# Performance work log

Hardware: AMD Instinct MI355X
Metric: run time of the kernel (lower is better)

Reference implementation:

```python
import jax, jax.numpy as jnp
import numpy as np

N, M, C = 32768, 8192, 128
K = 3            # number of interpolation neighbors (PointNet++/RepSurf FP)
EPS_BN = 1e-5    # torch BatchNorm1d default eps
EPS_D = 1e-8     # RepSurf dist_recip eps


def setup_inputs() -> dict:
    key = jax.random.key(0)
    ks = jax.random.split(key, 16)
    s = 0.05
    inp = {
        "pos1": jax.random.normal(ks[0], (N, 3), jnp.float32),
        "pos2": jax.random.normal(ks[1], (M, 3), jnp.float32),
        "feat2": jax.random.normal(ks[2], (M, C), jnp.float32),
    }
    # MLP stack [128,128,128]: Linear + BatchNorm1d (gamma/beta) per layer
    for i in range(3):
        inp[f"W{i}"] = jax.random.normal(ks[3 + i], (C, C), jnp.float32) * s
        inp[f"b{i}"] = jnp.zeros((C,), jnp.float32)
        inp[f"g{i}"] = jnp.ones((C,), jnp.float32)
        inp[f"be{i}"] = jnp.zeros((C,), jnp.float32)
    return inp


def _lin_bn_relu(x, W, b, g, be):
    # Linear -> BatchNorm1d (training-mode batch stats, biased var) -> ReLU
    y = x @ W.T + b
    m = y.mean(axis=0)
    v = y.var(axis=0)
    return jax.nn.relu((y - m) * jax.lax.rsqrt(v + EPS_BN) * g + be)


def reference(pos1, pos2, feat2, W0, b0, g0, be0, W1, b1, g1, be1, W2, b2, g2, be2):
    # squared pairwise distances [N, M] (memory-bound: 1 GB fp32)
    d = ((pos1 ** 2).sum(-1, keepdims=True)
         + (pos2 ** 2).sum(-1)[None, :]
         - 2.0 * (pos1 @ pos2.T))
    neg_d, idx = jax.lax.top_k(-d, K)          # 3 nearest neighbors
    dk = jnp.maximum(-neg_d, 0.0)              # [N, K] squared dists
    w = 1.0 / (dk + EPS_D)
    w = w / w.sum(-1, keepdims=True)           # inverse-distance weights
    # gather neighbor features and interpolate: [N, K, C] -> [N, C]
    interp = jnp.einsum('nkc,nk->nc', feat2[idx], w)
    x = _lin_bn_relu(interp, W0, b0, g0, be0)
    x = _lin_bn_relu(x, W1, b1, g1, be1)
    x = _lin_bn_relu(x, W2, b2, g2, be2)
    return x
```

## Files before the change

### kernel.cpp

```cpp
#include <hip/hip_runtime.h>
#include <math.h>

#define NQ 32768
#define MC 8192
#define CC 128
#define EPS_BN 1e-5f
#define EPS_D  1e-8

#define DBL_BIG 1e300
#define IDX_BIG 0x7fffffff

#define QB  64
#define TB  512
#define NW  8
#define HM  (MC / 2)
#define SLCW (HM / NW)
#define KMASK 0xFFFFE000u
#define IMASK 0x1FFFu
#define NSURV 64
#define KNN_B ((NQ / QB) * 2)
#define GEMM_B (NQ / 64)
#define NGRP 8

typedef __attribute__((ext_vector_type(8))) short bf16x8;
typedef __attribute__((ext_vector_type(4))) float floatx4;
typedef unsigned short ushort_t;

__device__ __forceinline__ unsigned bf16pair(float a, float b) {
    unsigned ua = __float_as_uint(a); ua = (ua + 0x7FFFu + ((ua >> 16) & 1u)) >> 16;
    unsigned ub = __float_as_uint(b); ub = (ub + 0x7FFFu + ((ub >> 16) & 1u)) >> 16;
    return ua | (ub << 16);
}
__device__ __forceinline__ ushort_t bf16one(float a) {
    unsigned ua = __float_as_uint(a);
    return (ushort_t)((ua + 0x7FFFu + ((ua >> 16) & 1u)) >> 16);
}
__device__ __forceinline__ float bflo(unsigned u) { return __uint_as_float(u << 16); }
__device__ __forceinline__ float bfhi(unsigned u) { return __uint_as_float(u & 0xFFFF0000u); }

__device__ __forceinline__ void ins4(float& k0, float& k1, float& k2, float& k3, float x) {
    const float n0 = fminf(k0, x);
    const float n1 = __builtin_amdgcn_fmed3f(k0, k1, x);
    const float n2 = __builtin_amdgcn_fmed3f(k1, k2, x);
    const float n3 = __builtin_amdgcn_fmed3f(k2, k3, x);
    k0 = n0; k1 = n1; k2 = n2; k3 = n3;
}

__device__ __forceinline__ float mkk(float nx, float ny, float nz, float hp,
                                     float4 c, unsigned j) {
    float t = c.w + hp;
    t = fmaf(nz, c.z, t);
    t = fmaf(ny, c.y, t);
    t = fmaf(nx, c.x, t);
    return __uint_as_float((__float_as_uint(t) & KMASK) | j);
}

__global__ __launch_bounds__(TB) void pack_kernel(const float* __restrict__ pos2,
                                                  float4* __restrict__ pos2pk) {
    const int c0 = blockIdx.x * (MC / 8);
#pragma unroll
    for (int c = c0 + threadIdx.x; c < c0 + MC / 8; c += TB) {
        const float x = pos2[c * 3 + 0];
        const float y = pos2[c * 3 + 1];
        const float z = pos2[c * 3 + 2];
        float4 v;
        v.x = x; v.y = y; v.z = z;
        v.w = 0.5f * fmaf(x, x, fmaf(y, y, z * z));
        pos2pk[c] = v;
    }
}

__global__ __launch_bounds__(TB) void knn_kernel(const float* __restrict__ pos1,
                                                 const float4* __restrict__ pos2pk,
                                                 unsigned* __restrict__ skeys,
                                                 const float* __restrict__ W0,
                                                 const float* __restrict__ W1,
                                                 const float* __restrict__ W2,
                                                 ushort_t* __restrict__ Wbf,
                                                 float* __restrict__ stats) {
    __shared__ unsigned skl[QB][33];

    if (blockIdx.x >= KNN_B) {
        const int pb = blockIdx.x - KNN_B;
        const int f = pb * TB + threadIdx.x;
        const float* Ws[3] = {W0, W1, W2};
#pragma unroll
        for (int l = 0; l < 3; ++l) {
            const float4 v = ((const float4*)Ws[l])[f];
            unsigned* dst = (unsigned*)(Wbf + (size_t)l * CC * CC);
            dst[f * 2 + 0] = bf16pair(v.x, v.y);
            dst[f * 2 + 1] = bf16pair(v.z, v.w);
        }
        if (pb == 0)
            for (int i = threadIdx.x; i < 3 * NGRP * 256; i += TB) stats[i] = 0.f;
        return;
    }

    const int half = blockIdx.x & 1;
    const int bq   = blockIdx.x >> 1;
    const int ln = threadIdx.x & 63;
    const int wvu = __builtin_amdgcn_readfirstlane((int)(threadIdx.x >> 6));
    const int q  = bq * QB + ln;

    const float px = pos1[q * 3 + 0];
    const float py = pos1[q * 3 + 1];
    const float pz = pos1[q * 3 + 2];
    const float nx = -px, ny = -py, nz = -pz;
    const float hp = 0.5f * fmaf(px, px, fmaf(py, py, pz * pz));

    const int jb = half * HM + wvu * SLCW;
    const float4* cp = pos2pk + jb;

    const float KINIT = __uint_as_float(0x7F000000u);
    float k0 = KINIT, k1 = KINIT, k2 = KINIT, k3 = KINIT;

#pragma unroll 4
    for (int gi = 0; gi < SLCW / 4; ++gi) {
        const float4 c0 = cp[gi * 4 + 0];
        const float4 c1 = cp[gi * 4 + 1];
        const float4 c2 = cp[gi * 4 + 2];
        const float4 c3 = cp[gi * 4 + 3];
        const unsigned j0 = (unsigned)(jb + gi * 4);
        ins4(k0, k1, k2, k3, mkk(nx, ny, nz, hp, c0, j0 + 0));
        ins4(k0, k1, k2, k3, mkk(nx, ny, nz, hp, c1, j0 + 1));
        ins4(k0, k1, k2, k3, mkk(nx, ny, nz, hp, c2, j0 + 2));
        ins4(k0, k1, k2, k3, mkk(nx, ny, nz, hp, c3, j0 + 3));
    }

    skl[ln][wvu * 4 + 0] = __float_as_uint(k0);
    skl[ln][wvu * 4 + 1] = __float_as_uint(k1);
    skl[ln][wvu * 4 + 2] = __float_as_uint(k2);
    skl[ln][wvu * 4 + 3] = __float_as_uint(k3);
    __syncthreads();

#pragma unroll
    for (int t = threadIdx.x * 4; t < threadIdx.x * 4 + 4; ++t) {
        const int ql = t >> 5, slot = t & 31;
        skeys[(size_t)(bq * QB + ql) * NSURV + half * 32 + slot] = skl[ql][slot];
    }
}

template <int MODE>
__global__ __launch_bounds__(256) void gemm_mfma(const void* __restrict__ Xsrc_,
                                                 const unsigned* __restrict__ skeys,
                                                 const float* __restrict__ pos1,
                                                 const float* __restrict__ pos2,
                                                 const float* __restrict__ statsIn,
                                                 const float* __restrict__ gIn,
                                                 const float* __restrict__ beIn,
                                                 const ushort_t* __restrict__ Wb,
                                                 const float* __restrict__ bias,
                                                 ushort_t* __restrict__ Y,
                                                 float* __restrict__ statsOut) {
    __shared__ __align__(16) short xa[64][136];
    __shared__ __align__(16) short wb[128][136];
    __shared__ float blk_s[CC], blk_q[CC];
    __shared__ float sc_l[CC], sh_l[CC];

    const int row0 = blockIdx.x * 64;

    if constexpr (MODE == 0) {
        const float* feat2 = (const float*)Xsrc_;
        __shared__ int   lidx[QB][3];
        __shared__ float lw[QB][3];
        {
            double* rrd = (double*)&xa[0][0];
            int*    rri = (int*)&wb[0][0];
            const int ql = threadIdx.x >> 2;
            const int pp = threadIdx.x & 3;
            const int qg = row0 + ql;
            const double qx = (double)pos1[qg * 3 + 0];
            const double qy = (double)pos1[qg * 3 + 1];
            const double qz = (double)pos1[qg * 3 + 2];
            double b0 = DBL_BIG, b1 = DBL_BIG, b2 = DBL_BIG;
            int    j0 = IDX_BIG, j1 = IDX_BIG, j2 = IDX_BIG;
            const uint4* kp = (const uint4*)(skeys + (size_t)qg * NSURV + pp * 16);
#pragma unroll
            for (int gi = 0; gi < 4; ++gi) {
                const uint4 kk = kp[gi];
                const unsigned ks[4] = {kk.x, kk.y, kk.z, kk.w};
#pragma unroll
                for (int u = 0; u < 4; ++u) {
                    const int id = (int)(ks[u] & IMASK);
                    const double x = (double)pos2[id * 3 + 0];
                    const double y = (double)pos2[id * 3 + 1];
                    const double z = (double)pos2[id * 3 + 2];
                    const double ax = qx - x, ay = qy - y, az = qz - z;
                    const double d = ax * ax + ay * ay + az * az;
                    const bool l2 = (d < b2) || (d == b2 && id < j2);
                    if (l2) {
                        const bool l1 = (d < b1) || (d == b1 && id < j1);
                        const bool l0 = (d < b0) || (d == b0 && id < j0);
                        b2 = l1 ? b1 : d;              j2 = l1 ? j1 : id;
                        b1 = l1 ? (l0 ? b0 : d) : b1;  j1 = l1 ? (l0 ? j0 : id) : j1;
                        b0 = l0 ? d : b0;              j0 = l0 ? id : j0;
                    }
                }
            }
            const int base = (ql * 4 + pp) * 3;
            rrd[base + 0] = b0; rri[base + 0] = j0;
            rrd[base + 1] = b1; rri[base + 1] = j1;
            rrd[base + 2] = b2; rri[base + 2] = j2;
            __syncthreads();
            if (threadIdx.x < QB) {
                const int qq = threadIdx.x;
                double c0 = DBL_BIG, c1 = DBL_BIG, c2 = DBL_BIG;
                int    i0 = IDX_BIG, i1 = IDX_BIG, i2 = IDX_BIG;
#pragma unroll
                for (int s = 0; s < 12; ++s) {
                    const double d = rrd[qq * 12 + s];
                    const int   id = rri[qq * 12 + s];
                    const bool l2 = (d < c2) || (d == c2 && id < i2);
                    if (l2) {
                        const bool l1 = (d < c1) || (d == c1 && id < i1);
                        const bool l0 = (d < c0) || (d == c0 && id < i0);
                        c2 = l1 ? c1 : d;              i2 = l1 ? i1 : id;
                        c1 = l1 ? (l0 ? c0 : d) : c1;  i1 = l1 ? (l0 ? i0 : id) : i1;
                        c0 = l0 ? d : c0;              i0 = l0 ? id : i0;
                    }
                }
                const double r0 = 1.0 / (c0 + EPS_D);
                const double r1 = 1.0 / (c1 + EPS_D);
                const double r2 = 1.0 / (c2 + EPS_D);
                const double inv = 1.0 / (r0 + r1 + r2);
                lidx[qq][0] = i0; lidx[qq][1] = i1; lidx[qq][2] = i2;
                lw[qq][0] = (float)(r0 * inv);
                lw[qq][1] = (float)(r1 * inv);
                lw[qq][2] = (float)(r2 * inv);
            }
            __syncthreads();
        }
        if (threadIdx.x < CC) { blk_s[threadIdx.x] = 0.f; blk_q[threadIdx.x] = 0.f; }
#pragma unroll
        for (int e = threadIdx.x; e < 64 * 32; e += 256) {
            const int r = e >> 5, c4 = e & 31;
            const int i0 = lidx[r][0], i1 = lidx[r][1], i2 = lidx[r][2];
            const float w0 = lw[r][0], w1 = lw[r][1], w2 = lw[r][2];
            const float4 f0 = *(const float4*)&feat2[(size_t)i0 * CC + c4 * 4];
            const float4 f1 = *(const float4*)&feat2[(size_t)i1 * CC + c4 * 4];
            const float4 f2 = *(const float4*)&feat2[(size_t)i2 * CC + c4 * 4];
            float4 v;
            v.x = w0 * f0.x + w1 * f1.x + w2 * f2.x;
            v.y = w0 * f0.y + w1 * f1.y + w2 * f2.y;
            v.z = w0 * f0.z + w1 * f1.z + w2 * f2.z;
            v.w = w0 * f0.w + w1 * f1.w + w2 * f2.w;
            unsigned* dst = (unsigned*)&xa[r][0];
            dst[c4 * 2 + 0] = bf16pair(v.x, v.y);
            dst[c4 * 2 + 1] = bf16pair(v.z, v.w);
        }
    } else {
        const ushort_t* Xbf = (const ushort_t*)Xsrc_;
        if (threadIdx.x < CC) {
            const int c = threadIdx.x;
            float s = 0.f, q = 0.f;
#pragma unroll
            for (int gr = 0; gr < NGRP; ++gr) {
                s += statsIn[gr * 256 + c];
                q += statsIn[gr * 256 + CC + c];
            }
            const float m = s * (1.f / (float)NQ);
            const float v = fmaf(-m, m, q * (1.f / (float)NQ));
            const float rstd = rsqrtf(v + EPS_BN);
            const float scl = gIn[c] * rstd;
            sc_l[c] = scl;
            sh_l[c] = fmaf(-m, scl, beIn[c]);
            blk_s[c] = 0.f; blk_q[c] = 0.f;
        }
        __syncthreads();
#pragma unroll
        for (int e = threadIdx.x; e < 64 * 16; e += 256) {
            const int r = e >> 4, c8 = e & 15;
            const uint4 u = *(const uint4*)&Xbf[(size_t)(row0 + r) * CC + c8 * 8];
            const float4 s0 = *(const float4*)&sc_l[c8 * 8];
            const float4 s1 = *(const float4*)&sc_l[c8 * 8 + 4];
            const float4 h0 = *(const float4*)&sh_l[c8 * 8];
            const float4 h1 = *(const float4*)&sh_l[c8 * 8 + 4];
            const float v0 = fmaxf(fmaf(bflo(u.x), s0.x, h0.x), 0.f);
            const float v1 = fmaxf(fmaf(bfhi(u.x), s0.y, h0.y), 0.f);
            const float v2 = fmaxf(fmaf(bflo(u.y), s0.z, h0.z), 0.f);
            const float v3 = fmaxf(fmaf(bfhi(u.y), s0.w, h0.w), 0.f);
            const float v4 = fmaxf(fmaf(bflo(u.z), s1.x, h1.x), 0.f);
            const float v5 = fmaxf(fmaf(bfhi(u.z), s1.y, h1.y), 0.f);
            const float v6 = fmaxf(fmaf(bflo(u.w), s1.z, h1.z), 0.f);
            const float v7 = fmaxf(fmaf(bfhi(u.w), s1.w, h1.w), 0.f);
            uint4 o;
            o.x = bf16pair(v0, v1); o.y = bf16pair(v2, v3);
            o.z = bf16pair(v4, v5); o.w = bf16pair(v6, v7);
            *(uint4*)&xa[r][c8 * 8] = o;
        }
    }
#pragma unroll
    for (int e = threadIdx.x; e < 128 * 16; e += 256) {
        const int co = e >> 4, seg = e & 15;
        *(float4*)&wb[co][seg * 8] = *(const float4*)&Wb[(size_t)co * CC + seg * 8];
    }
    __syncthreads();

    const int lane = threadIdx.x & 63;
    const int wv = threadIdx.x >> 6;
    const int nn = lane & 15;
    const int quad = lane >> 4;

    floatx4 acc[8] = {};

    const short* arow = &xa[wv * 16 + nn][0];
#pragma unroll
    for (int ks = 0; ks < 4; ++ks) {
        const bf16x8 a = *(const bf16x8*)(arow + ks * 32 + quad * 8);
#pragma unroll
        for (int ct = 0; ct < 8; ++ct) {
            const bf16x8 b = *(const bf16x8*)(&wb[ct * 16 + nn][0] + ks * 32 + quad * 8);
            acc[ct] = __builtin_amdgcn_mfma_f32_16x16x32_bf16(a, b, acc[ct], 0, 0, 0);
        }
    }

#pragma unroll
    for (int ct = 0; ct < 8; ++ct) {
        const float bv = bias[ct * 16 + nn];
        float s = 0.f, qv = 0.f;
#pragma unroll
        for (int r = 0; r < 4; ++r) {
            acc[ct][r] += bv;
            s += acc[ct][r];
            qv = fmaf(acc[ct][r], acc[ct][r], qv);
        }
#pragma unroll
        for (int r = 0; r < 4; ++r)
            Y[(size_t)(row0 + wv * 16 + quad * 4 + r) * CC + ct * 16 + nn] = bf16one(acc[ct][r]);
        s += __shfl_xor(s, 16, 64); s += __shfl_xor(s, 32, 64);
        qv += __shfl_xor(qv, 16, 64); qv += __shfl_xor(qv, 32, 64);
        if (quad == 0) {
            atomicAdd(&blk_s[ct * 16 + nn], s);
            atomicAdd(&blk_q[ct * 16 + nn], qv);
        }
    }
    __syncthreads();
    {
        const int ch = threadIdx.x;
        const float v = (ch < CC) ? blk_s[ch] : blk_q[ch - CC];
        atomicAdd(&statsOut[(blockIdx.x & (NGRP - 1)) * 256 + ch], v);
    }
}

__global__ __launch_bounds__(256) void bn_final(const ushort_t* __restrict__ Y,
                                                const float* __restrict__ statsIn,
                                                const float* __restrict__ g,
                                                const float* __restrict__ be,
                                                float* __restrict__ out) {
    __shared__ float sc_l[CC], sh_l[CC];
    if (threadIdx.x < CC) {
        const int c = threadIdx.x;
        float s = 0.f, q = 0.f;
#pragma unroll
        for (int gr = 0; gr < NGRP; ++gr) {
            s += statsIn[gr * 256 + c];
            q += statsIn[gr * 256 + CC + c];
        }
        const float m = s * (1.f / (float)NQ);
        const float v = fmaf(-m, m, q * (1.f / (float)NQ));
        const float rstd = rsqrtf(v + EPS_BN);
        const float scl = g[c] * rstd;
        sc_l[c] = scl;
        sh_l[c] = fmaf(-m, scl, be[c]);
    }
    __syncthreads();
    const int base = blockIdx.x * 1024 + threadIdx.x;
#pragma unroll
    for (int it = 0; it < 4; ++it) {
        const int i8 = base + it * 256;
        const int c8 = (i8 & 15) * 8;
        const uint4 u = *(const uint4*)&Y[(size_t)i8 * 8];
        const float4 s0 = *(const float4*)&sc_l[c8];
        const float4 s1 = *(const float4*)&sc_l[c8 + 4];
        const float4 h0 = *(const float4*)&sh_l[c8];
        const float4 h1 = *(const float4*)&sh_l[c8 + 4];
        float4 o0, o1;
        o0.x = fmaxf(fmaf(bflo(u.x), s0.x, h0.x), 0.f);
        o0.y = fmaxf(fmaf(bfhi(u.x), s0.y, h0.y), 0.f);
        o0.z = fmaxf(fmaf(bflo(u.y), s0.z, h0.z), 0.f);
        o0.w = fmaxf(fmaf(bfhi(u.y), s0.w, h0.w), 0.f);
        o1.x = fmaxf(fmaf(bflo(u.z), s1.x, h1.x), 0.f);
        o1.y = fmaxf(fmaf(bfhi(u.z), s1.y, h1.y), 0.f);
        o1.z = fmaxf(fmaf(bflo(u.w), s1.z, h1.z), 0.f);
        o1.w = fmaxf(fmaf(bfhi(u.w), s1.w, h1.w), 0.f);
        ((float4*)out)[i8 * 2 + 0] = o0;
        ((float4*)out)[i8 * 2 + 1] = o1;
    }
}

extern "C" void kernel_launch(void* const* d_in, const int* in_sizes, int n_in,
                              void* d_out, int out_size, void* d_ws, size_t ws_size,
                              hipStream_t stream) {
    (void)in_sizes; (void)n_in; (void)out_size; (void)ws_size;

    const float* pos1  = (const float*)d_in[0];
    const float* pos2  = (const float*)d_in[1];
    const float* feat2 = (const float*)d_in[2];
    const float* Wl[3]  = {(const float*)d_in[3], (const float*)d_in[7],  (const float*)d_in[11]};
    const float* bl[3]  = {(const float*)d_in[4], (const float*)d_in[8],  (const float*)d_in[12]};
    const float* gl[3]  = {(const float*)d_in[5], (const float*)d_in[9],  (const float*)d_in[13]};
    const float* bel[3] = {(const float*)d_in[6], (const float*)d_in[10], (const float*)d_in[14]};

    float* ws = (float*)d_ws;
    ushort_t* B0 = (ushort_t*)ws;
    ushort_t* B1 = B0 + (size_t)NQ * CC;
    unsigned* skeys = (unsigned*)(B1 + (size_t)NQ * CC);
    float* stats = (float*)(skeys + (size_t)NQ * NSURV);
    ushort_t* Wbf = (ushort_t*)(stats + 3 * NGRP * 256);
    float4* pos2pk = (float4*)(Wbf + 3 * CC * CC);

    float* st0 = stats + 0 * NGRP * 256;
    float* st1 = stats + 1 * NGRP * 256;
    float* st2 = stats + 2 * NGRP * 256;

    pack_kernel<<<8, TB, 0, stream>>>(pos2, pos2pk);
    knn_kernel<<<KNN_B + 8, TB, 0, stream>>>(pos1, pos2pk, skeys,
                                             Wl[0], Wl[1], Wl[2], Wbf, stats);
    gemm_mfma<0><<<GEMM_B, 256, 0, stream>>>(feat2, skeys, pos1, pos2,
                                             nullptr, nullptr, nullptr,
                                             Wbf + 0 * CC * CC, bl[0], B0, st0);
    gemm_mfma<1><<<GEMM_B, 256, 0, stream>>>(B0, nullptr, nullptr, nullptr,
                                             st0, gl[0], bel[0],
                                             Wbf + 1 * CC * CC, bl[1], B1, st1);
    gemm_mfma<1><<<GEMM_B, 256, 0, stream>>>(B1, nullptr, nullptr, nullptr,
                                             st1, gl[1], bel[1],
                                             Wbf + 2 * CC * CC, bl[2], B0, st2);
    bn_final<<<GEMM_B, 256, 0, stream>>>(B0, st2, gl[2], bel[2], (float*)d_out);
}
```

Baseline: 211.7 us.

## Split KNN scan into four pieces with top-3 per wave and prefetching

The candidate scan is split across four blocks per query group with four waves each, and each wave keeps a top-3 list instead of top-4, so every key costs one fewer med3. The loop is restructured to double-buffer candidate loads in registers, and the survivor count drops from 64 to 48, which shrinks both the key writes and the fp64 refinement loop in the first GEMM. Cutting to three survivors per wave reduces the slack for errors from the truncated keys, so near-tied neighbours are more likely to be missed. The prefetch reads past the end of each slice, which is why four zero padding entries are added after pos2pk.

```diff
diff --git a/kernel.cpp b/kernel.cpp
--- a/kernel.cpp
+++ b/kernel.cpp
@@ -11,14 +11,15 @@
 #define IDX_BIG 0x7fffffff
 
 #define QB  64
-#define TB  512
-#define NW  8
-#define HM  (MC / 2)
-#define SLCW (HM / NW)
+#define TB  256
+#define NW  4
+#define PCE (MC / 4)
+#define SLCW (PCE / NW)
+#define NG  (SLCW / 4)
 #define KMASK 0xFFFFE000u
 #define IMASK 0x1FFFu
-#define NSURV 64
-#define KNN_B ((NQ / QB) * 2)
+#define NSURV 48
+#define KNN_B ((NQ / QB) * 4)
 #define GEMM_B (NQ / 64)
 #define NGRP 8
 
@@ -38,12 +39,11 @@
 __device__ __forceinline__ float bflo(unsigned u) { return __uint_as_float(u << 16); }
 __device__ __forceinline__ float bfhi(unsigned u) { return __uint_as_float(u & 0xFFFF0000u); }
 
-__device__ __forceinline__ void ins4(float& k0, float& k1, float& k2, float& k3, float x) {
+__device__ __forceinline__ void ins3(float& k0, float& k1, float& k2, float x) {
     const float n0 = fminf(k0, x);
     const float n1 = __builtin_amdgcn_fmed3f(k0, k1, x);
     const float n2 = __builtin_amdgcn_fmed3f(k1, k2, x);
-    const float n3 = __builtin_amdgcn_fmed3f(k2, k3, x);
-    k0 = n0; k1 = n1; k2 = n2; k3 = n3;
+    k0 = n0; k1 = n1; k2 = n2;
 }
 
 __device__ __forceinline__ float mkk(float nx, float ny, float nz, float hp,
@@ -52,7 +52,8 @@
     t = fmaf(nz, c.z, t);
     t = fmaf(ny, c.y, t);
     t = fmaf(nx, c.x, t);
-    return __uint_as_float((__float_as_uint(t) & KMASK) | j);
+    const unsigned u = (__float_as_uint(t) & KMASK) | (j & ~KMASK);
+    return __uint_as_float(u);
 }
 
 __global__ __launch_bounds__(TB) void pack_kernel(const float* __restrict__ pos2,
@@ -68,6 +69,10 @@
         v.w = 0.5f * fmaf(x, x, fmaf(y, y, z * z));
         pos2pk[c] = v;
     }
+    if (blockIdx.x == 0 && threadIdx.x < 4) {
+        float4 zf; zf.x = 0.f; zf.y = 0.f; zf.z = 0.f; zf.w = 0.f;
+        pos2pk[MC + threadIdx.x] = zf;
+    }
 }
 
 __global__ __launch_bounds__(TB) void knn_kernel(const float* __restrict__ pos1,
@@ -78,7 +83,7 @@
                                                  const float* __restrict__ W2,
                                                  ushort_t* __restrict__ Wbf,
                                                  float* __restrict__ stats) {
-    __shared__ unsigned skl[QB][33];
+    __shared__ unsigned skl[QB][13];
 
     if (blockIdx.x >= KNN_B) {
         const int pb = blockIdx.x - KNN_B;
@@ -96,8 +101,8 @@
         return;
     }
 
-    const int half = blockIdx.x & 1;
-    const int bq   = blockIdx.x >> 1;
+    const int piece = blockIdx.x & 3;
+    const int bq    = blockIdx.x >> 2;
     const int ln = threadIdx.x & 63;
     const int wvu = __builtin_amdgcn_readfirstlane((int)(threadIdx.x >> 6));
     const int q  = bq * QB + ln;
@@ -108,35 +113,43 @@
     const float nx = -px, ny = -py, nz = -pz;
     const float hp = 0.5f * fmaf(px, px, fmaf(py, py, pz * pz));
 
-    const int jb = half * HM + wvu * SLCW;
+    const int jb = piece * PCE + wvu * SLCW;
     const float4* cp = pos2pk + jb;
 
     const float KINIT = __uint_as_float(0x7F000000u);
-    float k0 = KINIT, k1 = KINIT, k2 = KINIT, k3 = KINIT;
-
-#pragma unroll 4
-    for (int gi = 0; gi < SLCW / 4; ++gi) {
-        const float4 c0 = cp[gi * 4 + 0];
-        const float4 c1 = cp[gi * 4 + 1];
-        const float4 c2 = cp[gi * 4 + 2];
-        const float4 c3 = cp[gi * 4 + 3];
-        const unsigned j0 = (unsigned)(jb + gi * 4);
-        ins4(k0, k1, k2, k3, mkk(nx, ny, nz, hp, c0, j0 + 0));
-        ins4(k0, k1, k2, k3, mkk(nx, ny, nz, hp, c1, j0 + 1));
-        ins4(k0, k1, k2, k3, mkk(nx, ny, nz, hp, c2, j0 + 2));
-        ins4(k0, k1, k2, k3, mkk(nx, ny, nz, hp, c3, j0 + 3));
-    }
-
-    skl[ln][wvu * 4 + 0] = __float_as_uint(k0);
-    skl[ln][wvu * 4 + 1] = __float_as_uint(k1);
-    skl[ln][wvu * 4 + 2] = __float_as_uint(k2);
-    skl[ln][wvu * 4 + 3] = __float_as_uint(k3);
+    float k0 = KINIT, k1 = KINIT, k2 = KINIT;
+
+#define LOADG(v0, v1, v2, v3, g) { v0 = cp[(g)*4+0]; v1 = cp[(g)*4+1]; \
+                                   v2 = cp[(g)*4+2]; v3 = cp[(g)*4+3]; }
+#define CONSG(v0, v1, v2, v3, g) { const unsigned j0 = (unsigned)(jb + (g)*4); \
+        ins3(k0, k1, k2, mkk(nx, ny, nz, hp, v0, j0 + 0)); \
+        ins3(k0, k1, k2, mkk(nx, ny, nz, hp, v1, j0 + 1)); \
+        ins3(k0, k1, k2, mkk(nx, ny, nz, hp, v2, j0 + 2)); \
+        ins3(k0, k1, k2, mkk(nx, ny, nz, hp, v3, j0 + 3)); }
+
+    float4 A0, A1, A2, A3, B0, B1, B2, B3;
+    LOADG(A0, A1, A2, A3, 0);
+    for (int g = 0; g < NG; g += 2) {
+        LOADG(B0, B1, B2, B3, g + 1);
+        CONSG(A0, A1, A2, A3, g);
+        LOADG(A0, A1, A2, A3, g + 2);
+        CONSG(B0, B1, B2, B3, g + 1);
+    }
+#undef LOADG
+#undef CONSG
+
+    skl[ln][wvu * 3 + 0] = __float_as_uint(k0);
+    skl[ln][wvu * 3 + 1] = __float_as_uint(k1);
+    skl[ln][wvu * 3 + 2] = __float_as_uint(k2);
     __syncthreads();
 
-#pragma unroll
-    for (int t = threadIdx.x * 4; t < threadIdx.x * 4 + 4; ++t) {
-        const int ql = t >> 5, slot = t & 31;
-        skeys[(size_t)(bq * QB + ql) * NSURV + half * 32 + slot] = skl[ql][slot];
+    {
+        const int ql = threadIdx.x >> 2;
+        const int sp = (threadIdx.x & 3) * 3;
+        unsigned* dst = &skeys[(size_t)(bq * QB + ql) * NSURV + piece * 12 + sp];
+        dst[0] = skl[ql][sp + 0];
+        dst[1] = skl[ql][sp + 1];
+        dst[2] = skl[ql][sp + 2];
     }
 }
 
@@ -174,9 +187,9 @@
             const double qz = (double)pos1[qg * 3 + 2];
             double b0 = DBL_BIG, b1 = DBL_BIG, b2 = DBL_BIG;
             int    j0 = IDX_BIG, j1 = IDX_BIG, j2 = IDX_BIG;
-            const uint4* kp = (const uint4*)(skeys + (size_t)qg * NSURV + pp * 16);
-#pragma unroll
-            for (int gi = 0; gi < 4; ++gi) {
+            const uint4* kp = (const uint4*)(skeys + (size_t)qg * NSURV + pp * 12);
+#pragma unroll
+            for (int gi = 0; gi < 3; ++gi) {
                 const uint4 kk = kp[gi];
                 const unsigned ks[4] = {kk.x, kk.y, kk.z, kk.w};
 #pragma unroll
@@ -414,8 +427,8 @@
     float* st2 = stats + 2 * NGRP * 256;
 
     pack_kernel<<<8, TB, 0, stream>>>(pos2, pos2pk);
-    knn_kernel<<<KNN_B + 8, TB, 0, stream>>>(pos1, pos2pk, skeys,
-                                             Wl[0], Wl[1], Wl[2], Wbf, stats);
+    knn_kernel<<<KNN_B + 16, TB, 0, stream>>>(pos1, pos2pk, skeys,
+                                              Wl[0], Wl[1], Wl[2], Wbf, stats);
     gemm_mfma<0><<<GEMM_B, 256, 0, stream>>>(feat2, skeys, pos1, pos2,
                                              nullptr, nullptr, nullptr,
                                              Wbf + 0 * CC * CC, bl[0], B0, st0);
```

After: 203.3 us. 1.04x faster.

## Compute KNN distance candidates with fp16 MFMA using hi/lo split coordinates

Applied to the files above, without the earlier changes.

Moves the brute-force distance computation in the KNN kernel from scalar FMA onto MFMA f16 16x16x32 instructions. Coordinates and half-norms are split into fp16 hi/lo parts so the dot-product expansion keeps near-fp32 accuracy. Each lane now keeps a top-3 instead of a top-4 survivor list, which cuts the surviving candidates per query from 64 to 24 and shrinks the double-precision refinement in the first GEMM stage. The risk is that the fp16 split loses enough precision that a true neighbor drops out of the survivors. The ptile fetch at t+2/t+3 on the last loop iteration also reads past the end of the half's tile range.

```diff
diff --git a/kernel.cpp b/kernel.cpp
--- a/kernel.cpp
+++ b/kernel.cpp
@@ -1,4 +1,5 @@
 #include <hip/hip_runtime.h>
+#include <hip/hip_fp16.h>
 #include <math.h>
 
 #define NQ 32768
@@ -11,18 +12,17 @@
 #define IDX_BIG 0x7fffffff
 
 #define QB  64
-#define TB  512
-#define NW  8
-#define HM  (MC / 2)
-#define SLCW (HM / NW)
+#define TB  256
+#define NTIL 256
 #define KMASK 0xFFFFE000u
 #define IMASK 0x1FFFu
-#define NSURV 64
+#define NSURV 24
 #define KNN_B ((NQ / QB) * 2)
 #define GEMM_B (NQ / 64)
 #define NGRP 8
 
 typedef __attribute__((ext_vector_type(8))) short bf16x8;
+typedef __attribute__((ext_vector_type(8))) _Float16 half8;
 typedef __attribute__((ext_vector_type(4))) float floatx4;
 typedef unsigned short ushort_t;
 
@@ -38,47 +38,51 @@
 __device__ __forceinline__ float bflo(unsigned u) { return __uint_as_float(u << 16); }
 __device__ __forceinline__ float bfhi(unsigned u) { return __uint_as_float(u & 0xFFFF0000u); }
 
-__device__ __forceinline__ void ins4(float& k0, float& k1, float& k2, float& k3, float x) {
+__device__ __forceinline__ void ins3(float& k0, float& k1, float& k2, float x) {
     const float n0 = fminf(k0, x);
     const float n1 = __builtin_amdgcn_fmed3f(k0, k1, x);
     const float n2 = __builtin_amdgcn_fmed3f(k1, k2, x);
-    const float n3 = __builtin_amdgcn_fmed3f(k2, k3, x);
-    k0 = n0; k1 = n1; k2 = n2; k3 = n3;
-}
-
-__device__ __forceinline__ float mkk(float nx, float ny, float nz, float hp,
-                                     float4 c, unsigned j) {
-    float t = c.w + hp;
-    t = fmaf(nz, c.z, t);
-    t = fmaf(ny, c.y, t);
-    t = fmaf(nx, c.x, t);
-    return __uint_as_float((__float_as_uint(t) & KMASK) | j);
-}
+    k0 = n0; k1 = n1; k2 = n2;
+}
+
+#define PK2(a, b) ((unsigned)__half_as_ushort(a) | ((unsigned)__half_as_ushort(b) << 16))
 
 __global__ __launch_bounds__(TB) void pack_kernel(const float* __restrict__ pos2,
-                                                  float4* __restrict__ pos2pk) {
-    const int c0 = blockIdx.x * (MC / 8);
-#pragma unroll
-    for (int c = c0 + threadIdx.x; c < c0 + MC / 8; c += TB) {
-        const float x = pos2[c * 3 + 0];
-        const float y = pos2[c * 3 + 1];
-        const float z = pos2[c * 3 + 2];
-        float4 v;
-        v.x = x; v.y = y; v.z = z;
-        v.w = 0.5f * fmaf(x, x, fmaf(y, y, z * z));
-        pos2pk[c] = v;
-    }
+                                                  uint4* __restrict__ ptile) {
+    const int c = blockIdx.x * TB + threadIdx.x;
+    const float x = pos2[c * 3 + 0];
+    const float y = pos2[c * 3 + 1];
+    const float z = pos2[c * 3 + 2];
+    const __half chx = __float2half(x); const float fchx = __half2float(chx);
+    const __half chy = __float2half(y); const float fchy = __half2float(chy);
+    const __half chz = __float2half(z); const float fchz = __half2float(chz);
+    const __half clx = __float2half(x - fchx);
+    const __half cly = __float2half(y - fchy);
+    const __half clz = __float2half(z - fchz);
+    const double X = (double)fchx + (double)__half2float(clx);
+    const double Y = (double)fchy + (double)__half2float(cly);
+    const double Z = (double)fchz + (double)__half2float(clz);
+    const double hc = 0.5 * (X * X + Y * Y + Z * Z);
+    const __half hchi = __float2half((float)hc);
+    const __half hclo = __float2half((float)(hc - (double)__half2float(hchi)));
+    const __half one = __float2half(1.0f);
+    uint4 a0, a1;
+    a0.x = PK2(chx, chy); a0.y = PK2(chz, clx); a0.z = PK2(cly, clz); a0.w = PK2(chx, chy);
+    a1.x = PK2(chz, clx); a1.y = PK2(cly, clz); a1.z = PK2(hchi, hclo); a1.w = PK2(one, one);
+    const int t = c >> 4, m = c & 15;
+    ptile[(size_t)t * 32 + m]      = a0;
+    ptile[(size_t)t * 32 + 16 + m] = a1;
 }
 
 __global__ __launch_bounds__(TB) void knn_kernel(const float* __restrict__ pos1,
-                                                 const float4* __restrict__ pos2pk,
+                                                 const uint4* __restrict__ ptile,
                                                  unsigned* __restrict__ skeys,
                                                  const float* __restrict__ W0,
                                                  const float* __restrict__ W1,
                                                  const float* __restrict__ W2,
                                                  ushort_t* __restrict__ Wbf,
                                                  float* __restrict__ stats) {
-    __shared__ unsigned skl[QB][33];
+    __shared__ __align__(16) ushort_t qext[QB][16];
 
     if (blockIdx.x >= KNN_B) {
         const int pb = blockIdx.x - KNN_B;
@@ -98,45 +102,89 @@
 
     const int half = blockIdx.x & 1;
     const int bq   = blockIdx.x >> 1;
-    const int ln = threadIdx.x & 63;
-    const int wvu = __builtin_amdgcn_readfirstlane((int)(threadIdx.x >> 6));
-    const int q  = bq * QB + ln;
-
-    const float px = pos1[q * 3 + 0];
-    const float py = pos1[q * 3 + 1];
-    const float pz = pos1[q * 3 + 2];
-    const float nx = -px, ny = -py, nz = -pz;
-    const float hp = 0.5f * fmaf(px, px, fmaf(py, py, pz * pz));
-
-    const int jb = half * HM + wvu * SLCW;
-    const float4* cp = pos2pk + jb;
+
+    if (threadIdx.x < QB) {
+        const int qq = bq * QB + threadIdx.x;
+        const float x = pos1[qq * 3 + 0];
+        const float y = pos1[qq * 3 + 1];
+        const float z = pos1[qq * 3 + 2];
+        const __half phx = __float2half(x); const float fphx = __half2float(phx);
+        const __half phy = __float2half(y); const float fphy = __half2float(phy);
+        const __half phz = __float2half(z); const float fphz = __half2float(phz);
+        const __half plx = __float2half(x - fphx);
+        const __half ply = __float2half(y - fphy);
+        const __half plz = __float2half(z - fphz);
+        const double X = (double)fphx + (double)__half2float(plx);
+        const double Y = (double)fphy + (double)__half2float(ply);
+        const double Z = (double)fphz + (double)__half2float(plz);
+        const double hp = 0.5 * (X * X + Y * Y + Z * Z);
+        const __half hphi = __float2half((float)hp);
+        const __half hplo = __float2half((float)(hp - (double)__half2float(hphi)));
+        const ushort_t SG = 0x8000u;
+        const ushort_t nx = (ushort_t)(__half_as_ushort(phx) ^ SG);
+        const ushort_t ny = (ushort_t)(__half_as_ushort(phy) ^ SG);
+        const ushort_t nz = (ushort_t)(__half_as_ushort(phz) ^ SG);
+        const ushort_t mx = (ushort_t)(__half_as_ushort(plx) ^ SG);
+        const ushort_t my = (ushort_t)(__half_as_ushort(ply) ^ SG);
+        const ushort_t mz = (ushort_t)(__half_as_ushort(plz) ^ SG);
+        const ushort_t on = __half_as_ushort(__float2half(1.0f));
+        ushort_t* e = &qext[threadIdx.x][0];
+        e[0] = nx; e[1] = ny; e[2] = nz; e[3] = nx; e[4]  = ny; e[5]  = nz;
+        e[6] = mx; e[7] = my; e[8] = mz; e[9] = mx; e[10] = my; e[11] = mz;
+        e[12] = on; e[13] = on;
+        e[14] = __half_as_ushort(hphi); e[15] = __half_as_ushort(hplo);
+    }
+    __syncthreads();
+
+    const int lane = threadIdx.x & 63;
+    const int wv   = threadIdx.x >> 6;
+    const int cc   = lane & 15;
+    const int g    = lane >> 4;
+
+    uint4 bqu = {0u, 0u, 0u, 0u};
+    if (g < 2) bqu = *(const uint4*)&qext[wv * 16 + cc][g * 8];
+    const half8 bqh = *(const half8*)&bqu;
+
+    const uint4* lp = ptile + (size_t)(half * NTIL) * 32 + ((g & 1) * 16 + cc);
+#define LD(t) lp[(size_t)(t) * 32]
 
     const float KINIT = __uint_as_float(0x7F000000u);
-    float k0 = KINIT, k1 = KINIT, k2 = KINIT, k3 = KINIT;
-
-#pragma unroll 4
-    for (int gi = 0; gi < SLCW / 4; ++gi) {
-        const float4 c0 = cp[gi * 4 + 0];
-        const float4 c1 = cp[gi * 4 + 1];
-        const float4 c2 = cp[gi * 4 + 2];
-        const float4 c3 = cp[gi * 4 + 3];
-        const unsigned j0 = (unsigned)(jb + gi * 4);
-        ins4(k0, k1, k2, k3, mkk(nx, ny, nz, hp, c0, j0 + 0));
-        ins4(k0, k1, k2, k3, mkk(nx, ny, nz, hp, c1, j0 + 1));
-        ins4(k0, k1, k2, k3, mkk(nx, ny, nz, hp, c2, j0 + 2));
-        ins4(k0, k1, k2, k3, mkk(nx, ny, nz, hp, c3, j0 + 3));
-    }
-
-    skl[ln][wvu * 4 + 0] = __float_as_uint(k0);
-    skl[ln][wvu * 4 + 1] = __float_as_uint(k1);
-    skl[ln][wvu * 4 + 2] = __float_as_uint(k2);
-    skl[ln][wvu * 4 + 3] = __float_as_uint(k3);
-    __syncthreads();
-
-#pragma unroll
-    for (int t = threadIdx.x * 4; t < threadIdx.x * 4 + 4; ++t) {
-        const int ql = t >> 5, slot = t & 31;
-        skeys[(size_t)(bq * QB + ql) * NSURV + half * 32 + slot] = skl[ql][slot];
+    float k0 = KINIT, k1 = KINIT, k2 = KINIT;
+    unsigned j0 = (unsigned)(half * 4096 + g * 4 + 0);
+    unsigned j1 = j0 + 1, j2 = j0 + 2, j3 = j0 + 3;
+    const floatx4 zc = {0.f, 0.f, 0.f, 0.f};
+
+#define KEYS(d) { \
+        unsigned u0 = (__float_as_uint(d[0]) & KMASK) | (j0 & ~KMASK); \
+        unsigned u1 = (__float_as_uint(d[1]) & KMASK) | (j1 & ~KMASK); \
+        unsigned u2 = (__float_as_uint(d[2]) & KMASK) | (j2 & ~KMASK); \
+        unsigned u3 = (__float_as_uint(d[3]) & KMASK) | (j3 & ~KMASK); \
+        ins3(k0, k1, k2, __uint_as_float(u0)); \
+        ins3(k0, k1, k2, __uint_as_float(u1)); \
+        ins3(k0, k1, k2, __uint_as_float(u2)); \
+        ins3(k0, k1, k2, __uint_as_float(u3)); \
+        j0 += 16; j1 += 16; j2 += 16; j3 += 16; }
+
+    uint4 afA = LD(0);
+    uint4 afB = LD(1);
+    for (int t = 0; t < NTIL; t += 2) {
+        const uint4 nA = LD(t + 2);
+        const floatx4 dA = __builtin_amdgcn_mfma_f32_16x16x32_f16(*(const half8*)&afA, bqh, zc, 0, 0, 0);
+        KEYS(dA);
+        const uint4 nB = LD(t + 3);
+        const floatx4 dB = __builtin_amdgcn_mfma_f32_16x16x32_f16(*(const half8*)&afB, bqh, zc, 0, 0, 0);
+        KEYS(dB);
+        afA = nA; afB = nB;
+    }
+#undef LD
+#undef KEYS
+
+    {
+        const int q = bq * QB + wv * 16 + cc;
+        unsigned* dst = skeys + (size_t)q * NSURV + half * 12 + g * 3;
+        dst[0] = __float_as_uint(k0);
+        dst[1] = __float_as_uint(k1);
+        dst[2] = __float_as_uint(k2);
     }
 }
 
@@ -174,27 +222,24 @@
             const double qz = (double)pos1[qg * 3 + 2];
             double b0 = DBL_BIG, b1 = DBL_BIG, b2 = DBL_BIG;
             int    j0 = IDX_BIG, j1 = IDX_BIG, j2 = IDX_BIG;
-            const uint4* kp = (const uint4*)(skeys + (size_t)qg * NSURV + pp * 16);
-#pragma unroll
-            for (int gi = 0; gi < 4; ++gi) {
-                const uint4 kk = kp[gi];
-                const unsigned ks[4] = {kk.x, kk.y, kk.z, kk.w};
-#pragma unroll
-                for (int u = 0; u < 4; ++u) {
-                    const int id = (int)(ks[u] & IMASK);
-                    const double x = (double)pos2[id * 3 + 0];
-                    const double y = (double)pos2[id * 3 + 1];
-                    const double z = (double)pos2[id * 3 + 2];
-                    const double ax = qx - x, ay = qy - y, az = qz - z;
-                    const double d = ax * ax + ay * ay + az * az;
-                    const bool l2 = (d < b2) || (d == b2 && id < j2);
-                    if (l2) {
-                        const bool l1 = (d < b1) || (d == b1 && id < j1);
-                        const bool l0 = (d < b0) || (d == b0 && id < j0);
-                        b2 = l1 ? b1 : d;              j2 = l1 ? j1 : id;
-                        b1 = l1 ? (l0 ? b0 : d) : b1;  j1 = l1 ? (l0 ? j0 : id) : j1;
-                        b0 = l0 ? d : b0;              j0 = l0 ? id : j0;
-                    }
+            const uint2* kp = (const uint2*)(skeys + (size_t)qg * NSURV + pp * 6);
+            const uint2 ka = kp[0], kb = kp[1], kc = kp[2];
+            const unsigned ks[6] = {ka.x, ka.y, kb.x, kb.y, kc.x, kc.y};
+#pragma unroll
+            for (int u = 0; u < 6; ++u) {
+                const int id = (int)(ks[u] & IMASK);
+                const double x = (double)pos2[id * 3 + 0];
+                const double y = (double)pos2[id * 3 + 1];
+                const double z = (double)pos2[id * 3 + 2];
+                const double ax = qx - x, ay = qy - y, az = qz - z;
+                const double d = ax * ax + ay * ay + az * az;
+                const bool l2 = (d < b2) || (d == b2 && id < j2);
+                if (l2) {
+                    const bool l1 = (d < b1) || (d == b1 && id < j1);
+                    const bool l0 = (d < b0) || (d == b0 && id < j0);
+                    b2 = l1 ? b1 : d;              j2 = l1 ? j1 : id;
+                    b1 = l1 ? (l0 ? b0 : d) : b1;  j1 = l1 ? (l0 ? j0 : id) : j1;
+                    b0 = l0 ? d : b0;              j0 = l0 ? id : j0;
                 }
             }
             const int base = (ql * 4 + pp) * 3;
@@ -407,15 +452,15 @@
     unsigned* skeys = (unsigned*)(B1 + (size_t)NQ * CC);
     float* stats = (float*)(skeys + (size_t)NQ * NSURV);
     ushort_t* Wbf = (ushort_t*)(stats + 3 * NGRP * 256);
-    float4* pos2pk = (float4*)(Wbf + 3 * CC * CC);
+    uint4* ptile = (uint4*)(Wbf + 3 * CC * CC);
 
     float* st0 = stats + 0 * NGRP * 256;
     float* st1 = stats + 1 * NGRP * 256;
     float* st2 = stats + 2 * NGRP * 256;
 
-    pack_kernel<<<8, TB, 0, stream>>>(pos2, pos2pk);
-    knn_kernel<<<KNN_B + 8, TB, 0, stream>>>(pos1, pos2pk, skeys,
-                                             Wl[0], Wl[1], Wl[2], Wbf, stats);
+    pack_kernel<<<MC / TB, TB, 0, stream>>>(pos2, ptile);
+    knn_kernel<<<KNN_B + 16, TB, 0, stream>>>(pos1, ptile, skeys,
+                                              Wl[0], Wl[1], Wl[2], Wbf, stats);
     gemm_mfma<0><<<GEMM_B, 256, 0, stream>>>(feat2, skeys, pos1, pos2,
                                              nullptr, nullptr, nullptr,
                                              Wbf + 0 * CC * CC, bl[0], B0, st0);
```

Result: faster. 201.4 us (-4.9%).
